# Kernel tuning notes

Hardware: AMD Instinct MI355X
Metric: run time of the kernel (lower is better)

## Reference

```python
import jax, jax.numpy as jnp
import numpy as np

B, T0, H0, W0 = 16, 8, 14, 14
DIM = 768
HEADS = 8
HD = DIM // HEADS  # 96
N = T0 * H0 * W0 + 1  # 1569 (cls token)
STRIDE_Q = (1, 1, 1)
STRIDE_KV = (1, 2, 2)
REL_SP_DIM = 2 * max(H0, H0 // 2) - 1  # 27
REL_T_DIM = 2 * T0 - 1  # 15
LN_EPS = 1e-5


def _rel_idx(q, k):
    # decomposed relative-position index table (static, numpy)
    q_ratio = max(k / q, 1.0)
    k_ratio = max(q / k, 1.0)
    d = np.arange(q)[:, None] * q_ratio - np.arange(k)[None, :] * k_ratio
    d += (k - 1) * k_ratio
    return d.astype(np.int64)


def _layernorm(x, g, b):
    m = jnp.mean(x, axis=-1, keepdims=True)
    v = jnp.mean((x - m) ** 2, axis=-1, keepdims=True)
    return (x - m) * jax.lax.rsqrt(v + LN_EPS) * g + b


def _attention_pool(t, w, thw, stride, g, b):
    # t: [B, heads, 1+L, C]; depthwise 3x3x3 conv over THW, cls token bypasses pool
    cls_tok, body = t[:, :, :1], t[:, :, 1:]
    Bb, NH, L, C = body.shape
    T, H, W = thw
    x = body.reshape(Bb * NH, T, H, W, C).transpose(0, 4, 1, 2, 3)  # NCDHW
    y = jax.lax.conv_general_dilated(
        x, w, window_strides=stride, padding=[(1, 1), (1, 1), (1, 1)],
        feature_group_count=C, dimension_numbers=('NCDHW', 'OIDHW', 'NCDHW'))
    nT, nH, nW = y.shape[2], y.shape[3], y.shape[4]
    y = y.reshape(Bb, NH, C, nT * nH * nW).transpose(0, 1, 3, 2)
    y = jnp.concatenate([cls_tok, y], axis=2)
    return _layernorm(y, g, b), (nT, nH, nW)


def setup_inputs() -> dict:
    key = jax.random.key(0)
    ks = jax.random.split(key, 12)
    s = 0.02
    inp = {
        'x': jax.random.normal(ks[0], (B, N, DIM), jnp.float32),
        'qkv_w': jax.random.normal(ks[1], (DIM, 3 * DIM), jnp.float32) * s,
        'qkv_b': jax.random.normal(ks[2], (3 * DIM,), jnp.float32) * s,
        'pool_q_w': jax.random.normal(ks[3], (HD, 1, 3, 3, 3), jnp.float32) * s,
        'pool_k_w': jax.random.normal(ks[4], (HD, 1, 3, 3, 3), jnp.float32) * s,
        'pool_v_w': jax.random.normal(ks[5], (HD, 1, 3, 3, 3), jnp.float32) * s,
        'ln_q_g': jnp.ones((HD,), jnp.float32), 'ln_q_b': jnp.zeros((HD,), jnp.float32),
        'ln_k_g': jnp.ones((HD,), jnp.float32), 'ln_k_b': jnp.zeros((HD,), jnp.float32),
        'ln_v_g': jnp.ones((HD,), jnp.float32), 'ln_v_b': jnp.zeros((HD,), jnp.float32),
        'rel_pos_h': jax.random.normal(ks[6], (REL_SP_DIM, HD), jnp.float32) * s,
        'rel_pos_w': jax.random.normal(ks[7], (REL_SP_DIM, HD), jnp.float32) * s,
        'rel_pos_t': jax.random.normal(ks[8], (REL_T_DIM, HD), jnp.float32) * s,
        'proj_w': jax.random.normal(ks[9], (DIM, DIM), jnp.float32) * s,
        'proj_b': jax.random.normal(ks[10], (DIM,), jnp.float32) * s,
        'thw_t': T0, 'thw_h': H0, 'thw_w': W0,
    }
    return inp


def reference(x, qkv_w, qkv_b, pool_q_w, pool_k_w, pool_v_w,
              ln_q_g, ln_q_b, ln_k_g, ln_k_b, ln_v_g, ln_v_b,
              rel_pos_h, rel_pos_w, rel_pos_t, proj_w, proj_b,
              thw_t, thw_h, thw_w):
    thw = (int(thw_t), int(thw_h), int(thw_w))
    Bb, Nn, _ = x.shape
    qkv = (x @ qkv_w + qkv_b).reshape(Bb, Nn, 3, HEADS, HD).transpose(2, 0, 3, 1, 4)
    q, k, v = qkv[0], qkv[1], qkv[2]  # [B, H, N, hd]
    q, q_shape = _attention_pool(q, pool_q_w, thw, STRIDE_Q, ln_q_g, ln_q_b)
    k, k_shape = _attention_pool(k, pool_k_w, thw, STRIDE_KV, ln_k_g, ln_k_b)
    v, _ = _attention_pool(v, pool_v_w, thw, STRIDE_KV, ln_v_g, ln_v_b)
    qt, qh, qw = q_shape
    kt, kh, kw = k_shape
    scale = HD ** -0.5
    attn = jnp.einsum('bhqc,bhkc->bhqk', q * scale, k)  # [B,H,1+Lq,1+Lk]
    # spatial + temporal decomposed relative position bias (cls row/col excluded)
    Rh = rel_pos_h[_rel_idx(qh, kh)]  # [qh,kh,hd]
    Rw = rel_pos_w[_rel_idx(qw, kw)]  # [qw,kw,hd]
    Rt = rel_pos_t[_rel_idx(qt, kt)]  # [qt,kt,hd]
    r_q = q[:, :, 1:].reshape(Bb, HEADS, qt, qh, qw, HD)
    rel_h = jnp.einsum('bythwc,hkc->bythwk', r_q, Rh)  # [B,H,qt,qh,qw,kh]
    rel_w = jnp.einsum('bythwc,wkc->bythwk', r_q, Rw)  # [B,H,qt,qh,qw,kw]
    rel_t = jnp.einsum('bnthwc,tkc->bnthwk', r_q, Rt)  # [B,H,qt,qh,qw,kt]
    bias = (rel_h[:, :, :, :, :, None, :, None]
            + rel_w[:, :, :, :, :, None, None, :]
            + rel_t[:, :, :, :, :, :, None, None])  # [B,H,qt,qh,qw,kt,kh,kw]
    attn = attn.at[:, :, 1:, 1:].add(bias.reshape(Bb, HEADS, qt * qh * qw, kt * kh * kw))
    attn = jax.nn.softmax(attn, axis=-1)
    out = jnp.einsum('bhqk,bhkc->bhqc', attn, v)
    out = out.at[:, :, 1:].add(q[:, :, 1:])  # residual pooling (skip cls)
    out = out.transpose(0, 2, 1, 3).reshape(Bb, -1, DIM)
    out = out @ proj_w + proj_b
    return out
```

## Files before the change

kernel.cpp:

```cpp
#include <hip/hip_runtime.h>
#include <hip/hip_bf16.h>

typedef __hip_bfloat16 bf16;
typedef __attribute__((ext_vector_type(8))) short bf16x8;
typedef __attribute__((ext_vector_type(4))) float f32x4;

#define B_     16
#define N_     1569
#define DIM_   768
#define NHEADS 8
#define HD_    96
#define LK_    393
#define T0_    8
#define H0_    14
#define W0_    14

struct __align__(8) bf16x4s { bf16 a, b, c, d; };

__device__ __forceinline__ float b2f(unsigned short u) {
  union { unsigned int i; float f; } x;
  x.i = ((unsigned int)u) << 16;
  return x.f;
}

__global__ __launch_bounds__(256) void cvt_f32_bf16(
    const float* __restrict__ in, bf16* __restrict__ out, int n4) {
  int i = blockIdx.x * 256 + threadIdx.x;
  if (i < n4) {
    float4 v = ((const float4*)in)[i];
    bf16x4s o{__float2bfloat16(v.x), __float2bfloat16(v.y),
              __float2bfloat16(v.z), __float2bfloat16(v.w)};
    ((bf16x4s*)out)[i] = o;
  }
}

__global__ __launch_bounds__(256) void transpose_f32_bf16(
    const float* __restrict__ in, bf16* __restrict__ out, int R, int C) {
  __shared__ float tile[32][33];
  int c0 = blockIdx.x * 32, r0 = blockIdx.y * 32;
  int tx = threadIdx.x, ty = threadIdx.y;
  for (int i = 0; i < 32; i += 8) {
    int r = r0 + ty + i, c = c0 + tx;
    if (r < R && c < C) tile[ty + i][tx] = in[(size_t)r * C + c];
  }
  __syncthreads();
  for (int i = 0; i < 32; i += 8) {
    int c = c0 + ty + i, r = r0 + tx;
    if (c < C && r < R) out[(size_t)c * R + r] = __float2bfloat16(tile[tx][ty + i]);
  }
}

__global__ __launch_bounds__(256) void prep_pw(
    const float* __restrict__ wq, const float* __restrict__ wk,
    const float* __restrict__ wv, float* __restrict__ outp) {
  int i = blockIdx.x * 256 + threadIdx.x;
  if (i < 2592) {
    int widx = i / 96, x = i % 96;
    outp[i]        = wq[x * 27 + widx];
    outp[2592 + i] = wk[x * 27 + widx];
    outp[5184 + i] = wv[x * 27 + widx];
  }
}

__device__ __forceinline__ void gl_lds16(const bf16* g, bf16* l) {
  __builtin_amdgcn_global_load_lds(
      (const __attribute__((address_space(1))) void*)g,
      (__attribute__((address_space(3))) void*)l, 16, 0, 0);
}

template <typename OutT>
__global__ __launch_bounds__(256) void gemm_bt(
    const bf16* __restrict__ A, const bf16* __restrict__ BT,
    const float* __restrict__ bias, OutT* __restrict__ C,
    int M, int Nn, int K) {
  constexpr int BM = 128, BN = 128, BK = 64;
  __shared__ __align__(16) bf16 As[BM][BK];
  __shared__ __align__(16) bf16 Bs[BN][BK];
  const int tid = threadIdx.x;
  const int lane = tid & 63, wave = tid >> 6;

  const int nNp = Nn >> 7;
  const int nwg = gridDim.x;
  const int q8 = nwg >> 3, r8 = nwg & 7;
  const int xcd = blockIdx.x & 7, idx = blockIdx.x >> 3;
  const int w = (xcd < r8 ? xcd * (q8 + 1) : r8 * (q8 + 1) + (xcd - r8) * q8) + idx;
  const int bm = (w / nNp) * BM, bn = (w % nNp) * BN;

  const int wm = (wave >> 1) * 64, wn = (wave & 1) * 64;
  const int sl = lane >> 3;
  const int sc = ((lane & 7) ^ sl) * 8;

  f32x4 acc[4][4];
#pragma unroll
  for (int i = 0; i < 4; ++i)
#pragma unroll
    for (int j = 0; j < 4; ++j) acc[i][j] = (f32x4){0.f, 0.f, 0.f, 0.f};

  for (int k0 = 0; k0 < K; k0 += BK) {
#pragma unroll
    for (int c = 0; c < 4; ++c) {
      int r0 = wave * 32 + c * 8;
      int arow = bm + r0 + sl;
      if (arow >= M) arow = M - 1;
      gl_lds16(A + (size_t)arow * K + k0 + sc, &As[r0][0]);
      int brow = bn + r0 + sl;
      gl_lds16(BT + (size_t)brow * K + k0 + sc, &Bs[r0][0]);
    }
    __syncthreads();
    const int fr = lane & 15, q = lane >> 4;
#pragma unroll
    for (int ks = 0; ks < 2; ++ks) {
      const int ph = (((ks << 2) + q) ^ (fr & 7)) << 3;
      bf16x8 af[4], bfr[4];
#pragma unroll
      for (int i = 0; i < 4; ++i) {
        af[i] = *(const bf16x8*)&As[wm + i * 16 + fr][ph];
        bfr[i] = *(const bf16x8*)&Bs[wn + i * 16 + fr][ph];
      }
#pragma unroll
      for (int i = 0; i < 4; ++i)
#pragma unroll
        for (int j = 0; j < 4; ++j)
          acc[i][j] = __builtin_amdgcn_mfma_f32_16x16x32_bf16(af[i], bfr[j],
                                                              acc[i][j], 0, 0, 0);
    }
    __syncthreads();
  }

  const int fr = lane & 15, rg = (lane >> 4) * 4;
#pragma unroll
  for (int j = 0; j < 4; ++j) {
    int col = bn + wn + j * 16 + fr;
    float bv = bias[col];
#pragma unroll
    for (int i = 0; i < 4; ++i) {
#pragma unroll
      for (int r = 0; r < 4; ++r) {
        int row = bm + wm + i * 16 + rg + r;
        if (row < M)
          C[(size_t)row * Nn + col] = (OutT)(acc[i][j][r] + bv);
      }
    }
  }
}

__global__ __launch_bounds__(256) void pool_ln(
    const bf16* __restrict__ qkv, const float* __restrict__ pwT,
    const float* __restrict__ g, const float* __restrict__ bt,
    bf16* __restrict__ outp, int which, int sHW, int oH, int oW, int Lout) {
  __shared__ float pwl[27 * 104];
  const int tid = threadIdx.x;
  for (int i = tid; i < 2592; i += 256) {
    int widx = i / 96, c = i % 96;
    int cgi = c >> 3, j = c & 7;
    pwl[widx * 104 + cgi * 8 + (cgi >> 2) * 4 + j] = pwT[i];
  }
  __syncthreads();

  const int rloc = tid >> 4;
  const int cg = tid & 15;
  const int orow = blockIdx.x * 16 + rloc;
  if (orow >= Lout) return;
  const int bh = blockIdx.y;
  const int b = bh >> 3, h = bh & 7;
  const bool act = (cg < 12);
  const bf16* base =
      qkv + (size_t)b * N_ * 2304 + which * 768 + h * 96 + cg * 8;

  float acc[8];
#pragma unroll
  for (int j = 0; j < 8; ++j) acc[j] = 0.f;

  if (act) {
    if (orow == 0) {
      union { uint4 u; bf16 e[8]; } tv;
      tv.u = *(const uint4*)base;
#pragma unroll
      for (int j = 0; j < 8; ++j) acc[j] = (float)tv.e[j];
    } else {
      int pos = orow - 1;
      int ot = pos / (oH * oW), r = pos % (oH * oW);
      int oh = r / oW, ow = r % oW;
      const float* wrow = pwl + cg * 8 + (cg >> 2) * 4;
#pragma unroll
      for (int kt = 0; kt < 3; ++kt) {
        int it = ot + kt - 1;
        if (it < 0 || it >= T0_) continue;
#pragma unroll
        for (int kh = 0; kh < 3; ++kh) {
          int ih = oh * sHW + kh - 1;
          if (ih < 0 || ih >= H0_) continue;
#pragma unroll
          for (int kw = 0; kw < 3; ++kw) {
            int iw = ow * sHW + kw - 1;
            if (iw < 0 || iw >= W0_) continue;
            int n = 1 + (it * H0_ + ih) * W0_ + iw;
            int widx = (kt * 3 + kh) * 3 + kw;
            union { uint4 u; bf16 e[8]; } tv;
            tv.u = *(const uint4*)(base + (size_t)n * 2304);
            const float* w = wrow + widx * 104;
            float wv_[8];
            *(float4*)&wv_[0] = *(const float4*)w;
            *(float4*)&wv_[4] = *(const float4*)(w + 4);
#pragma unroll
            for (int j = 0; j < 8; ++j) acc[j] += (float)tv.e[j] * wv_[j];
          }
        }
      }
    }
  }

  float s = 0.f, s2 = 0.f;
#pragma unroll
  for (int j = 0; j < 8; ++j) { s += acc[j]; s2 += acc[j] * acc[j]; }
#pragma unroll
  for (int mk = 1; mk < 16; mk <<= 1) {
    s += __shfl_xor(s, mk);
    s2 += __shfl_xor(s2, mk);
  }
  float mean = s * (1.f / 96.f);
  float var = s2 * (1.f / 96.f) - mean * mean;
  float rstd = rsqrtf(var + 1e-5f);

  if (act) {
    float gv[8], bv[8];
    *(float4*)&gv[0] = *(const float4*)(g + cg * 8);
    *(float4*)&gv[4] = *(const float4*)(g + cg * 8 + 4);
    *(float4*)&bv[0] = *(const float4*)(bt + cg * 8);
    *(float4*)&bv[4] = *(const float4*)(bt + cg * 8 + 4);
    union { uint4 u; bf16 e[8]; } ov;
#pragma unroll
    for (int j = 0; j < 8; ++j)
      ov.e[j] = __float2bfloat16((acc[j] - mean) * rstd * gv[j] + bv[j]);
    *(uint4*)(outp + ((size_t)bh * Lout + orow) * 96 + cg * 8) = ov.u;
  }
}

__global__ __launch_bounds__(256) void rel_dots(
    const bf16* __restrict__ qp, const float* __restrict__ rpt,
    const float* __restrict__ rph, const float* __restrict__ rpw,
    float* __restrict__ relq) {
  __shared__ float tab[69 * 100];
  __shared__ __align__(16) bf16 Qls[64][96];
  const int tid = threadIdx.x;
  const int bh = blockIdx.y;
  const int q0 = blockIdx.x * 64;
  const bf16* qb = qp + (size_t)bh * N_ * HD_;

  for (int i = tid; i < 69 * 24; i += 256) {
    int row = i / 24, c4 = (i % 24) * 4;
    const float* src = row < 15 ? rpt + row * 96
                      : row < 42 ? rph + (row - 15) * 96
                                 : rpw + (row - 42) * 96;
    *(float4*)&tab[row * 100 + c4] = *(const float4*)(src + c4);
  }
  for (int c = tid; c < 768; c += 256) {
    int row = c / 12, seg = c % 12;
    int p = q0 + row;
    if (p >= N_) p = N_ - 1;
    *(uint4*)&Qls[row][seg * 8] = *(const uint4*)(qb + (size_t)p * HD_ + seg * 8);
  }
  __syncthreads();

  const int r8 = tid >> 5, slot = tid & 31;
  if (slot == 15 || slot >= 23) return;
  for (int g = 0; g < 8; ++g) {
    int row = g * 8 + r8;
    int p = q0 + row;
    if (p < 1 || p >= N_) continue;
    int pos = p - 1;
    int qt = pos / 196, rr = pos % 196;
    int qh = rr / 14, qw = rr % 14;
    int ti = slot < 8 ? qt - slot + 7
            : slot < 15 ? 15 + (qh - 2 * (slot - 8) + 12)
                        : 42 + (qw - 2 * (slot - 16) + 12);
    const float* trow = &tab[ti * 100];
    float acc = 0.f;
#pragma unroll
    for (int d4 = 0; d4 < 24; ++d4) {
      float4 w = *(const float4*)(trow + d4 * 4);
      union { uint2 u; unsigned short s[4]; } qv;
      qv.u = *(const uint2*)&Qls[row][d4 * 4];
      acc += w.x * b2f(qv.s[0]) + w.y * b2f(qv.s[1]) +
             w.z * b2f(qv.s[2]) + w.w * b2f(qv.s[3]);
    }
    relq[((size_t)bh * N_ + p) * 24 + slot] = acc;
  }
}

__global__ __launch_bounds__(256) void attn_fused(
    const bf16* __restrict__ qp, const bf16* __restrict__ kp,
    const bf16* __restrict__ vp, const float* __restrict__ relq,
    bf16* __restrict__ aout) {
  __shared__ __align__(16) bf16 Ks[64][104];
  __shared__ __align__(16) bf16 VtS[96 * 64];
  __shared__ __align__(16) bf16 Ps[4][16][72];
  __shared__ float relb[64][24];

  const int tid = threadIdx.x;
  const int wv = tid >> 6, lane = tid & 63;
  const int col = lane & 15, quad = lane >> 4;
  const int bh = blockIdx.y;
  const int b = bh >> 3;
  const int h = bh & 7;
  const int q0 = blockIdx.x * 64;
  const bf16* qb = qp + (size_t)bh * N_ * HD_;
  const bf16* kb = kp + (size_t)bh * LK_ * HD_;
  const bf16* vb = vp + (size_t)bh * LK_ * HD_;
  const float scale = 0.102062072615966f;

  {
    int nrow = N_ - q0;
    if (nrow > 64) nrow = 64;
    int n4 = nrow * 6;
    const uint4* src = (const uint4*)(relq + ((size_t)bh * N_ + q0) * 24);
    for (int i = tid; i < n4; i += 256) ((uint4*)relb)[i] = src[i];
  }

  int qrow = q0 + wv * 16 + col;
  if (qrow >= N_) qrow = N_ - 1;
  bf16x8 qa[3];
#pragma unroll
  for (int ks_ = 0; ks_ < 3; ++ks_)
    qa[ks_] = *(const bf16x8*)(qb + (size_t)qrow * HD_ + ks_ * 32 + quad * 8);

  float mrun[4] = {-1e30f, -1e30f, -1e30f, -1e30f};
  float lrun[4] = {0.f, 0.f, 0.f, 0.f};
  f32x4 oacc[6];
#pragma unroll
  for (int dt = 0; dt < 6; ++dt) oacc[dt] = (f32x4){0.f, 0.f, 0.f, 0.f};

  for (int kt_i = 0; kt_i < 7; ++kt_i) {
    const int kt0 = kt_i * 64;
    __syncthreads();
    for (int c = tid; c < 768; c += 256) {
      int row = c / 12, seg = c % 12;
      int key = kt0 + row;
      if (key >= LK_) key = LK_ - 1;
      *(uint4*)&Ks[row][seg * 8] =
          *(const uint4*)(kb + (size_t)key * HD_ + seg * 8);
      union { uint4 u; bf16 e[8]; } tv;
      tv.u = *(const uint4*)(vb + (size_t)key * HD_ + seg * 8);
#pragma unroll
      for (int j = 0; j < 8; ++j) {
        int d = seg * 8 + j;
        int c_ = (d ^ (d >> 3)) & 7;
        VtS[d * 64 + (row ^ (c_ << 3))] = tv.e[j];
      }
    }
    __syncthreads();

    f32x4 sacc[4];
#pragma unroll
    for (int jt = 0; jt < 4; ++jt) sacc[jt] = (f32x4){0.f, 0.f, 0.f, 0.f};
#pragma unroll
    for (int ks_ = 0; ks_ < 3; ++ks_) {
#pragma unroll
      for (int jt = 0; jt < 4; ++jt) {
        bf16x8 bk = *(const bf16x8*)&Ks[jt * 16 + col][ks_ * 32 + quad * 8];
        sacc[jt] = __builtin_amdgcn_mfma_f32_16x16x32_bf16(qa[ks_], bk, sacc[jt], 0, 0, 0);
      }
    }

    float sv[4][4];
#pragma unroll
    for (int jt = 0; jt < 4; ++jt) {
      int kglob = kt0 + jt * 16 + col;
      bool kvalid = (kglob < LK_);
      int kbod = (kglob >= 1) ? kglob - 1 : 0;
      int kt_ = kbod / 49, krem = kbod % 49;
      int kh_ = krem / 7, kw_ = krem % 7;
#pragma unroll
      for (int r = 0; r < 4; ++r) {
        int qr = wv * 16 + quad * 4 + r;
        int p = q0 + qr;
        float s = sacc[jt][r] * scale;
        if (kvalid && kglob >= 1 && p >= 1 && p < N_)
          s += relb[qr][kt_] + relb[qr][8 + kh_] + relb[qr][16 + kw_];
        if (!kvalid) s = -1e30f;
        sv[jt][r] = s;
      }
    }

    float pexp[4][4];
#pragma unroll
    for (int r = 0; r < 4; ++r) {
      float pm = fmaxf(fmaxf(sv[0][r], sv[1][r]), fmaxf(sv[2][r], sv[3][r]));
#pragma unroll
      for (int mk = 1; mk < 16; mk <<= 1) pm = fmaxf(pm, __shfl_xor(pm, mk));
      float mn = fmaxf(mrun[r], pm);
      float alpha = __expf(mrun[r] - mn);
      mrun[r] = mn;
      float rs = 0.f;
#pragma unroll
      for (int jt = 0; jt < 4; ++jt) {
        float e = __expf(sv[jt][r] - mn);
        pexp[jt][r] = e;
        rs += e;
      }
#pragma unroll
      for (int mk = 1; mk < 16; mk <<= 1) rs += __shfl_xor(rs, mk);
      lrun[r] = lrun[r] * alpha + rs;
#pragma unroll
      for (int dt = 0; dt < 6; ++dt) {
        oacc[dt][r] *= alpha;
      }
    }

#pragma unroll
    for (int jt = 0; jt < 4; ++jt)
#pragma unroll
      for (int r = 0; r < 4; ++r)
        Ps[wv][quad * 4 + r][jt * 16 + col] = __float2bfloat16(pexp[jt][r]);

#pragma unroll
    for (int ks_ = 0; ks_ < 2; ++ks_) {
      bf16x8 ap = *(const bf16x8*)&Ps[wv][col][ks_ * 32 + quad * 8];
#pragma unroll
      for (int dt = 0; dt < 6; ++dt) {
        int d = dt * 16 + col;
        int c_ = (d ^ (d >> 3)) & 7;
        bf16x8 bv =
            *(const bf16x8*)&VtS[d * 64 + ((ks_ * 32 + quad * 8) ^ (c_ << 3))];
        oacc[dt] = __builtin_amdgcn_mfma_f32_16x16x32_bf16(ap, bv, oacc[dt], 0, 0, 0);
      }
    }
  }

#pragma unroll
  for (int r = 0; r < 4; ++r) {
    int qr = wv * 16 + quad * 4 + r;
    int p = q0 + qr;
    if (p >= N_) continue;
    float inv = 1.f / lrun[r];
#pragma unroll
    for (int dt = 0; dt < 6; ++dt) {
      int d = dt * 16 + col;
      float val = oacc[dt][r] * inv;
      if (p >= 1) val += (float)qb[(size_t)p * HD_ + d];
      aout[((size_t)b * N_ + p) * DIM_ + h * HD_ + d] = __float2bfloat16(val);
    }
  }
}

extern "C" void kernel_launch(void* const* d_in, const int* in_sizes, int n_in,
                              void* d_out, int out_size, void* d_ws,
                              size_t ws_size, hipStream_t stream) {
  (void)in_sizes; (void)n_in; (void)out_size; (void)ws_size;
  const float* x      = (const float*)d_in[0];
  const float* qkv_w  = (const float*)d_in[1];
  const float* qkv_b  = (const float*)d_in[2];
  const float* pool_q = (const float*)d_in[3];
  const float* pool_k = (const float*)d_in[4];
  const float* pool_v = (const float*)d_in[5];
  const float* ln_q_g = (const float*)d_in[6];
  const float* ln_q_b = (const float*)d_in[7];
  const float* ln_k_g = (const float*)d_in[8];
  const float* ln_k_b = (const float*)d_in[9];
  const float* ln_v_g = (const float*)d_in[10];
  const float* ln_v_b = (const float*)d_in[11];
  const float* rph    = (const float*)d_in[12];
  const float* rpw    = (const float*)d_in[13];
  const float* rpt    = (const float*)d_in[14];
  const float* proj_w = (const float*)d_in[15];
  const float* proj_b = (const float*)d_in[16];

  char* ws = (char*)d_ws;
  bf16* wt_qkv  = (bf16*)(ws);
  bf16* wt_proj = (bf16*)(ws + 3538944);
  bf16* xb      = (bf16*)(ws + 4718592);
  bf16* aout    = xb;
  bf16* qkv     = (bf16*)(ws + 43278336);
  float* relq   = (float*)(ws + 43278336);
  bf16* qpoolb  = (bf16*)(ws + 158957568);
  bf16* kpoolb  = (bf16*)(ws + 197517312);
  bf16* vpoolb  = (bf16*)(ws + 207175680);
  float* pwT    = (float*)(ws + 216834048);
  float* outp   = (float*)d_out;

  int n4 = (B_ * N_ * DIM_) / 4;
  cvt_f32_bf16<<<(n4 + 255) / 256, 256, 0, stream>>>(x, xb, n4);
  transpose_f32_bf16<<<dim3(72, 24), dim3(32, 8), 0, stream>>>(qkv_w, wt_qkv, 768, 2304);
  transpose_f32_bf16<<<dim3(24, 24), dim3(32, 8), 0, stream>>>(proj_w, wt_proj, 768, 768);
  prep_pw<<<11, 256, 0, stream>>>(pool_q, pool_k, pool_v, pwT);

  gemm_bt<bf16><<<197 * 18, 256, 0, stream>>>(xb, wt_qkv, qkv_b, qkv,
                                              B_ * N_, 3 * DIM_, DIM_);

  pool_ln<<<dim3(99, 128), 256, 0, stream>>>(qkv, pwT, ln_q_g, ln_q_b, qpoolb,
                                             0, 1, 14, 14, N_);
  pool_ln<<<dim3(25, 128), 256, 0, stream>>>(qkv, pwT + 2592, ln_k_g, ln_k_b,
                                             kpoolb, 1, 2, 7, 7, LK_);
  pool_ln<<<dim3(25, 128), 256, 0, stream>>>(qkv, pwT + 5184, ln_v_g, ln_v_b,
                                             vpoolb, 2, 2, 7, 7, LK_);

  rel_dots<<<dim3(25, 128), 256, 0, stream>>>(qpoolb, rpt, rph, rpw, relq);

  attn_fused<<<dim3(25, 128), 256, 0, stream>>>(qpoolb, kpoolb, vpoolb, relq,
                                                aout);

  gemm_bt<float><<<197 * 6, 256, 0, stream>>>(aout, wt_proj, proj_b, outp,
                                              B_ * N_, DIM_, DIM_);
}
```

Before: 794.2 us.

## Pre-transpose pooled V in a separate kernel and alias attention shared memory

Adds a vtran kernel that writes pooled V transposed (head-dim major, keys padded to 448) to workspace, so attn_fused loads V^T tiles with vectorized 16-byte reads instead of scattering eight scalar bf16 stores per load into LDS. The P staging buffer now aliases the K tile region, with an extra barrier before P is written, which cuts shared memory per block and may raise occupancy. The cost is an extra kernel launch, an extra global round trip for V, and one more barrier per key tile.

```diff
diff --git a/kernel.cpp b/kernel.cpp
--- a/kernel.cpp
+++ b/kernel.cpp
@@ -233,6 +233,30 @@
     for (int j = 0; j < 8; ++j)
       ov.e[j] = __float2bfloat16((acc[j] - mean) * rstd * gv[j] + bv[j]);
     *(uint4*)(outp + ((size_t)bh * Lout + orow) * 96 + cg * 8) = ov.u;
+  }
+}
+
+__global__ __launch_bounds__(256) void vtran(
+    const bf16* __restrict__ vp, bf16* __restrict__ vt) {
+  __shared__ __align__(16) bf16 tile[64][104];
+  const int tid = threadIdx.x;
+  const int bh = blockIdx.y, kt0 = blockIdx.x * 64;
+  const bf16* src = vp + (size_t)bh * LK_ * HD_;
+  for (int c = tid; c < 768; c += 256) {
+    int row = c / 12, seg = c % 12;
+    int key = kt0 + row;
+    uint4 v = {0u, 0u, 0u, 0u};
+    if (key < LK_) v = *(const uint4*)(src + (size_t)key * HD_ + seg * 8);
+    *(uint4*)&tile[row][seg * 8] = v;
+  }
+  __syncthreads();
+  bf16* dst = vt + (size_t)bh * 96 * 448 + kt0;
+  for (int c = tid; c < 768; c += 256) {
+    int d = c >> 3, ch = c & 7;
+    union { uint4 u; bf16 e[8]; } o;
+#pragma unroll
+    for (int j = 0; j < 8; ++j) o.e[j] = tile[ch * 8 + j][d];
+    *(uint4*)(dst + (size_t)d * 448 + ch * 8) = o.u;
   }
 }
 
@@ -290,12 +314,13 @@
 
 __global__ __launch_bounds__(256) void attn_fused(
     const bf16* __restrict__ qp, const bf16* __restrict__ kp,
-    const bf16* __restrict__ vp, const float* __restrict__ relq,
+    const bf16* __restrict__ vtb, const float* __restrict__ relq,
     bf16* __restrict__ aout) {
-  __shared__ __align__(16) bf16 Ks[64][104];
-  __shared__ __align__(16) bf16 VtS[96 * 64];
-  __shared__ __align__(16) bf16 Ps[4][16][72];
-  __shared__ float relb[64][24];
+  __shared__ __align__(16) char smem[31744];
+  bf16 (*Ks)[104]    = (bf16(*)[104])smem;
+  bf16* VtS          = (bf16*)(smem + 13312);
+  float (*relb)[24]  = (float(*)[24])(smem + 25600);
+  bf16 (*Ps)[16][72] = (bf16(*)[16][72])smem;
 
   const int tid = threadIdx.x;
   const int wv = tid >> 6, lane = tid & 63;
@@ -306,7 +331,7 @@
   const int q0 = blockIdx.x * 64;
   const bf16* qb = qp + (size_t)bh * N_ * HD_;
   const bf16* kb = kp + (size_t)bh * LK_ * HD_;
-  const bf16* vb = vp + (size_t)bh * LK_ * HD_;
+  const bf16* vt = vtb + (size_t)bh * 96 * 448;
   const float scale = 0.102062072615966f;
 
   {
@@ -339,14 +364,12 @@
       if (key >= LK_) key = LK_ - 1;
       *(uint4*)&Ks[row][seg * 8] =
           *(const uint4*)(kb + (size_t)key * HD_ + seg * 8);
-      union { uint4 u; bf16 e[8]; } tv;
-      tv.u = *(const uint4*)(vb + (size_t)key * HD_ + seg * 8);
-#pragma unroll
-      for (int j = 0; j < 8; ++j) {
-        int d = seg * 8 + j;
-        int c_ = (d ^ (d >> 3)) & 7;
-        VtS[d * 64 + (row ^ (c_ << 3))] = tv.e[j];
-      }
+    }
+    for (int c = tid; c < 768; c += 256) {
+      int d = c >> 3, ch = c & 7;
+      int c_ = (d ^ (d >> 3)) & 7;
+      *(uint4*)&VtS[d * 64 + ch * 8] =
+          *(const uint4*)(vt + (size_t)d * 448 + kt0 + ((ch ^ c_) * 8));
     }
     __syncthreads();
 
@@ -406,6 +429,8 @@
         oacc[dt][r] *= alpha;
       }
     }
+
+    __syncthreads();
 
 #pragma unroll
     for (int jt = 0; jt < 4; ++jt)
@@ -472,6 +497,7 @@
   bf16* aout    = xb;
   bf16* qkv     = (bf16*)(ws + 43278336);
   float* relq   = (float*)(ws + 43278336);
+  bf16* vtb     = (bf16*)(ws + 63278336);
   bf16* qpoolb  = (bf16*)(ws + 158957568);
   bf16* kpoolb  = (bf16*)(ws + 197517312);
   bf16* vpoolb  = (bf16*)(ws + 207175680);
@@ -494,9 +520,10 @@
   pool_ln<<<dim3(25, 128), 256, 0, stream>>>(qkv, pwT + 5184, ln_v_g, ln_v_b,
                                              vpoolb, 2, 2, 7, 7, LK_);
 
+  vtran<<<dim3(7, 128), 256, 0, stream>>>(vpoolb, vtb);
   rel_dots<<<dim3(25, 128), 256, 0, stream>>>(qpoolb, rpt, rph, rpw, relq);
 
-  attn_fused<<<dim3(25, 128), 256, 0, stream>>>(qpoolb, kpoolb, vpoolb, relq,
+  attn_fused<<<dim3(25, 128), 256, 0, stream>>>(qpoolb, kpoolb, vtb, relq,
                                                 aout);
 
   gemm_bt<float><<<197 * 6, 256, 0, stream>>>(aout, wt_proj, proj_b, outp,
```

Result: slower. 827.2 us (+4.2%).
